# Optimization experiments

Hardware: AMD Instinct MI355X
Metric: run time of the kernel (lower is better)

## Reference

```python
import jax, jax.numpy as jnp
import numpy as np
import itertools

# ---- fixed problem dims ----
B, C, G, D, H, W_SP = 2, 32, 24, 24, 24, 24   # octahedral group |G| = 24 (isomorphic to S4)
N_SEL = 3                                      # selective bispectrum: 2nd shift restricted to {e, transposition, 4-cycle}
FEAT = G * N_SEL                               # 72 invariant features per channel
HEAD = 64


def _octahedral_tables():
    """Cayley table of the octahedral rotation group (== S4) and the selective generator set."""
    perms = list(itertools.permutations(range(4)))          # lexicographic; identity at index 0
    idx = {p: i for i, p in enumerate(perms)}
    # cayley[i, j] = index of p_i o p_j, with (p o q)(k) = p(q(k))
    cay = np.array([[idx[tuple(p[q[k]] for k in range(4))] for q in perms] for p in perms],
                   dtype=np.int32)
    sel = np.array([idx[(0, 1, 2, 3)],   # identity
                    idx[(1, 0, 2, 3)],   # transposition (generator)
                    idx[(1, 2, 3, 0)]],  # 4-cycle (generator)
                   dtype=np.int32)
    return cay, sel


def setup_inputs() -> dict:
    key = jax.random.key(0)
    k1, k2, k3 = jax.random.split(key, 3)
    x = jax.random.normal(k1, (B, C, G, D, H, W_SP), dtype=jnp.float32)
    cay, sel = _octahedral_tables()
    # 1x1x1 Conv3d params: weight (HEAD, C*FEAT), bias (HEAD,)
    fan_in = C * FEAT
    W = jax.random.normal(k2, (HEAD, fan_in), dtype=jnp.float32) * (1.0 / np.sqrt(fan_in))
    b = jax.random.normal(k3, (HEAD,), dtype=jnp.float32) * 0.01
    return {"x": x, "W": W, "b": b,
            "cayley": jnp.asarray(cay), "sel_idx": jnp.asarray(sel)}


def _bispectrum_pool(x, W, b, cayley, sel_idx):
    Bb, Cc, Gg, Dd, Hh, Ww = x.shape
    # (B,C,G,D,H,W) -> rows of group signals, one per (b,c,voxel)
    xf = x.astype(jnp.float32).transpose(0, 1, 3, 4, 5, 2).reshape(-1, Gg)   # (N, 24)
    N = xf.shape[0]
    # Selective triple correlation (bispectrum in group domain):
    #   tau[n, h, s] = sum_g f(g) * f(g.h) * f(g.s),  s in selective generator set
    tau = jnp.zeros((N, Gg, N_SEL), dtype=jnp.float32)
    for g in range(Gg):                      # fixed small loop over 24 group elements
        row = cayley[g]                      # (24,) indices of g.h for all h
        fgh = xf[:, row]                     # (N, 24)
        fgs = fgh[:, sel_idx]                # (N, 3)
        tau = tau + xf[:, g][:, None, None] * fgh[:, :, None] * fgs[:, None, :]
    beta = tau.reshape(N, FEAT)              # real part of the bispectrum
    # sign * log1p compression
    out = jnp.sign(beta) * jnp.log1p(jnp.abs(beta))
    # (N, FEAT) -> (B, C*FEAT, D, H, W), channel index = c*FEAT + f (matches torch permute/reshape)
    out = out.reshape(Bb, Cc, Dd, Hh, Ww, FEAT).transpose(0, 1, 5, 2, 3, 4)
    out = out.reshape(Bb, Cc * FEAT, Dd, Hh, Ww)
    out = jax.nn.relu(out)
    # 1x1x1 conv == per-voxel GEMM
    y = jnp.einsum('bkdhw,ok->bodhw', out, W) + b[None, :, None, None, None]
    return y


def reference(x, W, b, cayley, sel_idx):
    return _bispectrum_pool(x, W, b, cayley, sel_idx)
```

## Files before the change

kernel.cpp:

```cpp
#include <hip/hip_runtime.h>
#include <stdint.h>

#define DHW         13824
#define NCH         32
#define NG          24
#define KDIM        2304
#define NHEAD       64
#define TP          16
#define CHS         16
#define FPC         64
#define KP2         2048
#define KS2         64
#define KPSTG       32
#define KQ          8
#define RPE         1024
#define TILES_PER_B 864
#define NTILES      1728
#define OUTN        1769472
#define WS_WBS      294912
#define WS_NEED     (WS_WBS + 2u * OUTN * 4u)

typedef __attribute__((ext_vector_type(2))) float    f32x2;
typedef __attribute__((ext_vector_type(8))) short    s16x8;
typedef __attribute__((ext_vector_type(4))) float    f32x4;
typedef __attribute__((ext_vector_type(4))) uint32_t u32x4;

struct Tables { int cay[NG][NG]; int s1[NG]; int s2[NG]; int t1h[NG]; int rep[12]; };

constexpr Tables make_tables() {
    int perms[NG][4] = {};
    int n = 0;
    for (int a = 0; a < 4; ++a)
        for (int b = 0; b < 4; ++b) {
            if (b == a) continue;
            for (int c = 0; c < 4; ++c) {
                if (c == a || c == b) continue;
                int d = 6 - a - b - c;
                perms[n][0] = a; perms[n][1] = b; perms[n][2] = c; perms[n][3] = d;
                ++n;
            }
        }
    int si1 = 0, si2 = 0;
    for (int i = 0; i < NG; ++i) {
        if (perms[i][0] == 1 && perms[i][1] == 0 && perms[i][2] == 2 && perms[i][3] == 3) si1 = i;
        if (perms[i][0] == 1 && perms[i][1] == 2 && perms[i][2] == 3 && perms[i][3] == 0) si2 = i;
    }
    Tables t{};
    for (int p = 0; p < NG; ++p) {
        for (int q = 0; q < NG; ++q) {
            int c0 = perms[p][perms[q][0]];
            int c1 = perms[p][perms[q][1]];
            int c2 = perms[p][perms[q][2]];
            int c3 = perms[p][perms[q][3]];
            int r = 0;
            for (int i = 0; i < NG; ++i)
                if (perms[i][0] == c0 && perms[i][1] == c1 &&
                    perms[i][2] == c2 && perms[i][3] == c3) { r = i; break; }
            t.cay[p][q] = r;
        }
        t.s1[p] = t.cay[p][si1];
        t.s2[p] = t.cay[p][si2];
    }
    for (int h = 0; h < NG; ++h) t.t1h[h] = t.cay[si1][h];
    int nr = 0;
    for (int h = 0; h < NG; ++h) if (h < t.t1h[h]) t.rep[nr++] = h;
    return t;
}
constexpr Tables TAB = make_tables();

__device__ __forceinline__ uint32_t f2bf(float f) {
    uint32_t u = __float_as_uint(f);
    u += 0x7fffu + ((u >> 16) & 1u);
    return u >> 16;
}

__global__ __launch_bounds__(256) void prep_w(const float* __restrict__ W,
                                              unsigned short* __restrict__ WbS) {
    int i = blockIdx.x * 256 + threadIdx.x;
    int j  = i & 7;
    int t1_ = i >> 3;
    int l  = t1_ & 63;
    int t2_ = t1_ >> 6;
    int kk = t2_ & (KS2 - 1);
    int ot = t2_ >> 6;
    int o = ot * 16 + (l & 15);
    int k = kk * 32 + ((l >> 4) << 3) + j;
    int stage = k >> 10;
    int q     = k & 1023;
    int c = stage * CHS + (q >> 6);
    int f = q & 63;
    const float* Wo = W + o * KDIM + c * 72;
    float val = 0.f;
    if (f < 24)      val = Wo[f * 3 + 0];
    else if (f < 36) { int h = TAB.rep[f - 24]; val = Wo[h * 3 + 1] + Wo[TAB.t1h[h] * 3 + 1]; }
    else if (f < 60) { int h = f - 36;          val = Wo[h * 3 + 2]; }
    WbS[i] = (unsigned short)f2bf(val * 0.69314718055994531f);
}

__global__ __launch_bounds__(256) void reduce_y(const float* __restrict__ part,
                                                const float* __restrict__ bias,
                                                float* __restrict__ y) {
    const int i4 = blockIdx.x * 256 + threadIdx.x;
    const f32x4 v0 = ((const f32x4*)part)[i4];
    const f32x4 v1 = ((const f32x4*)(part + OUTN))[i4];
    const float b  = bias[((i4 * 4) / DHW) & (NHEAD - 1)];
    f32x4 r = v0 + v1;
    r[0] += b; r[1] += b; r[2] += b; r[3] += b;
    ((f32x4*)y)[i4] = r;
}

template<int SPLIT>
__global__ __launch_bounds__(256, 2)
void bispec_fused(
        const float* __restrict__ x,
        const unsigned short* __restrict__ WbS,
        const float* __restrict__ bias,
        float* __restrict__ out)
{
    __shared__ alignas(16) unsigned short featS[TP * RPE];

    const int bid = blockIdx.x;
    const int NB  = SPLIT ? NTILES * 2 : NTILES;
    const int swz   = (bid & 7) * (NB / 8) + (bid >> 3);
    const int tile  = SPLIT ? (swz % NTILES) : swz;
    const int sbeg  = SPLIT ? (swz / NTILES) : 0;
    const int send  = SPLIT ? sbeg + 1 : 2;
    const int bb  = tile / TILES_PER_B;
    const int psp = (tile - bb * TILES_PER_B) * TP;
    const int tid = threadIdx.x;

    const int p0 = tid & 15;
    const int cl = tid >> 4;
    const int w  = tid >> 6;
    const int l  = tid & 63;
    const int ln = l & 15;
    const int lh = l >> 4;

    f32x4 accA = {0.f, 0.f, 0.f, 0.f};
    f32x4 accB = {0.f, 0.f, 0.f, 0.f};
    f32x4 accC = {0.f, 0.f, 0.f, 0.f};
    f32x4 accD = {0.f, 0.f, 0.f, 0.f};

    #pragma unroll 1
    for (int stage = sbeg; stage < send; ++stage) {
        {
            const int c0 = stage * CHS + cl;
            const unsigned idx0 = (unsigned)(bb * NCH + c0) * (NG * DHW) + (unsigned)(psp + p0);
            float xf[NG];
            #pragma unroll
            for (int g = 0; g < NG; ++g) xf[g] = x[idx0 + (unsigned)(g * DHW)];

            f32x2 tau02[NG];
            float tau1[12];
            #pragma unroll
            for (int h = 0; h < NG; ++h) tau02[h] = (f32x2){0.f, 0.f};
            #pragma unroll
            for (int r = 0; r < 12; ++r) tau1[r] = 0.f;
            #pragma unroll
            for (int g = 0; g < NG; ++g) {
                const float xg = xf[g];
                const f32x2 q02 = (f32x2){xg, xg} * (f32x2){xg, xf[TAB.s2[g]]};
                const float q1 = xg * xf[TAB.s1[g]];
                #pragma unroll
                for (int h = 0; h < NG; ++h) {
                    const float v = xf[TAB.cay[g][h]];
                    tau02[h] = __builtin_elementwise_fma((f32x2){v, v}, q02, tau02[h]);
                }
                #pragma unroll
                for (int r = 0; r < 12; ++r) {
                    const float v = xf[TAB.cay[g][TAB.rep[r]]];
                    tau1[r] = fmaf(q1, v, tau1[r]);
                }
            }
            uint32_t pk[FPC / 2];
            #pragma unroll
            for (int i = 0; i < 12; ++i) {
                float a = __log2f(1.f + fmaxf(tau02[2*i][0],   0.f));
                float b = __log2f(1.f + fmaxf(tau02[2*i+1][0], 0.f));
                pk[i] = f2bf(a) | (f2bf(b) << 16);
            }
            #pragma unroll
            for (int i = 0; i < 6; ++i) {
                float a = __log2f(1.f + fmaxf(tau1[2*i],   0.f));
                float b = __log2f(1.f + fmaxf(tau1[2*i+1], 0.f));
                pk[12 + i] = f2bf(a) | (f2bf(b) << 16);
            }
            #pragma unroll
            for (int i = 0; i < 12; ++i) {
                float a = __log2f(1.f + fmaxf(tau02[2*i][1],   0.f));
                float b = __log2f(1.f + fmaxf(tau02[2*i+1][1], 0.f));
                pk[18 + i] = f2bf(a) | (f2bf(b) << 16);
            }
            pk[30] = 0u; pk[31] = 0u;
            uint32_t* rowb = (uint32_t*)featS + p0 * (RPE / 2);
            #pragma unroll
            for (int j = 0; j < 8; ++j) {
                u32x4 v; v[0] = pk[j*4]; v[1] = pk[j*4+1]; v[2] = pk[j*4+2]; v[3] = pk[j*4+3];
                *(u32x4*)(rowb + ((((cl << 3) + j) ^ (p0 & 7)) << 2)) = v;
            }
        }
        __syncthreads();

        {
            const unsigned kb = (unsigned)(stage * KPSTG + w * KQ);
            const unsigned short* rowr = featS + ln * RPE;
            const int sx = ln & 7;
            const s16x8* wb = (const s16x8*)WbS;

            s16x8 bc = *(const s16x8*)(rowr + (((w * 32 + lh) ^ sx) << 3));
            #pragma unroll
            for (int kk = 0; kk < KQ; ++kk) {
                s16x8 bn = bc;
                if (kk + 1 < KQ)
                    bn = *(const s16x8*)(rowr + (((w * 32 + (kk + 1) * 4 + lh) ^ sx) << 3));
                const unsigned ai = (kb + (unsigned)kk) * 64u + (unsigned)l;
                s16x8 a0 = wb[ai];
                s16x8 a1 = wb[ai + 1u * KS2 * 64u];
                s16x8 a2 = wb[ai + 2u * KS2 * 64u];
                s16x8 a3 = wb[ai + 3u * KS2 * 64u];
                accA = __builtin_amdgcn_mfma_f32_16x16x32_bf16(a0, bc, accA, 0, 0, 0);
                accB = __builtin_amdgcn_mfma_f32_16x16x32_bf16(a1, bc, accB, 0, 0, 0);
                accC = __builtin_amdgcn_mfma_f32_16x16x32_bf16(a2, bc, accC, 0, 0, 0);
                accD = __builtin_amdgcn_mfma_f32_16x16x32_bf16(a3, bc, accD, 0, 0, 0);
                bc = bn;
            }
        }
        __syncthreads();
    }

    f32x4* redS = (f32x4*)featS;
    redS[(w * 4 + 0) * 64 + l] = accA;
    redS[(w * 4 + 1) * 64 + l] = accB;
    redS[(w * 4 + 2) * 64 + l] = accC;
    redS[(w * 4 + 3) * 64 + l] = accD;
    __syncthreads();
    f32x4 r = redS[(0 * 4 + w) * 64 + l] + redS[(1 * 4 + w) * 64 + l]
            + redS[(2 * 4 + w) * 64 + l] + redS[(3 * 4 + w) * 64 + l];

    const size_t obase = (SPLIT ? (size_t)sbeg * OUTN : 0)
                       + (size_t)bb * NHEAD * DHW + (size_t)(psp + ln);
    #pragma unroll
    for (int j = 0; j < 4; ++j) {
        const int o = w * 16 + lh * 4 + j;
        const float bv = SPLIT ? 0.f : bias[o];
        out[obase + (size_t)o * DHW] = r[j] + bv;
    }
}

extern "C" void kernel_launch(void* const* d_in, const int* in_sizes, int n_in,
                              void* d_out, int out_size, void* d_ws, size_t ws_size,
                              hipStream_t stream) {
    const float* x    = (const float*)d_in[0];
    const float* W    = (const float*)d_in[1];
    const float* bias = (const float*)d_in[2];
    unsigned short* WbS = (unsigned short*)d_ws;
    float* part = (float*)((char*)d_ws + WS_WBS);

    prep_w<<<dim3(NHEAD * KP2 / 256), dim3(256), 0, stream>>>(W, WbS);
    if (ws_size >= (size_t)WS_NEED) {
        bispec_fused<1><<<dim3(NTILES * 2), dim3(256), 0, stream>>>(x, WbS, bias, part);
        reduce_y<<<dim3(OUTN / 4 / 256), dim3(256), 0, stream>>>(part, bias, (float*)d_out);
    } else {
        bispec_fused<0><<<dim3(NTILES), dim3(256), 0, stream>>>(x, WbS, bias, (float*)d_out);
    }
}
```

Before: 62.15 us.

## Split channels four ways with half-group threads and atomic output accumulation

```diff
diff --git a/kernel.cpp b/kernel.cpp
--- a/kernel.cpp
+++ b/kernel.cpp
@@ -7,18 +7,18 @@
 #define KDIM        2304
 #define NHEAD       64
 #define TP          16
-#define CHS         16
+#define CHS         8
+#define NSTG        4
 #define FPC         64
 #define KP2         2048
 #define KS2         64
-#define KPSTG       32
-#define KQ          8
-#define RPE         1024
+#define KSTG        16
+#define KQ          4
+#define RPE         512
 #define TILES_PER_B 864
 #define NTILES      1728
+#define NB          (NTILES * NSTG)
 #define OUTN        1769472
-#define WS_WBS      294912
-#define WS_NEED     (WS_WBS + 2u * OUTN * 4u)
 
 typedef __attribute__((ext_vector_type(2))) float    f32x2;
 typedef __attribute__((ext_vector_type(8))) short    s16x8;
@@ -85,148 +85,147 @@
     int ot = t2_ >> 6;
     int o = ot * 16 + (l & 15);
     int k = kk * 32 + ((l >> 4) << 3) + j;
-    int stage = k >> 10;
-    int q     = k & 1023;
-    int c = stage * CHS + (q >> 6);
-    int f = q & 63;
+    int c  = k >> 6;
+    int f  = k & 63;
+    int H  = f >> 5, fl = f & 31;
     const float* Wo = W + o * KDIM + c * 72;
     float val = 0.f;
-    if (f < 24)      val = Wo[f * 3 + 0];
-    else if (f < 36) { int h = TAB.rep[f - 24]; val = Wo[h * 3 + 1] + Wo[TAB.t1h[h] * 3 + 1]; }
-    else if (f < 60) { int h = f - 36;          val = Wo[h * 3 + 2]; }
+    if (fl < 12)      val = Wo[(H * 12 + fl) * 3 + 0];
+    else if (fl < 18) { int h = TAB.rep[H * 6 + fl - 12];
+                        val = Wo[h * 3 + 1] + Wo[TAB.t1h[h] * 3 + 1]; }
+    else if (fl < 30) val = Wo[(H * 12 + fl - 18) * 3 + 2];
     WbS[i] = (unsigned short)f2bf(val * 0.69314718055994531f);
 }
 
-__global__ __launch_bounds__(256) void reduce_y(const float* __restrict__ part,
-                                                const float* __restrict__ bias,
-                                                float* __restrict__ y) {
+__global__ __launch_bounds__(256) void bias_add(float* __restrict__ y,
+                                                const float* __restrict__ bias) {
     const int i4 = blockIdx.x * 256 + threadIdx.x;
-    const f32x4 v0 = ((const f32x4*)part)[i4];
-    const f32x4 v1 = ((const f32x4*)(part + OUTN))[i4];
-    const float b  = bias[((i4 * 4) / DHW) & (NHEAD - 1)];
-    f32x4 r = v0 + v1;
-    r[0] += b; r[1] += b; r[2] += b; r[3] += b;
-    ((f32x4*)y)[i4] = r;
-}
-
-template<int SPLIT>
+    f32x4 v = ((f32x4*)y)[i4];
+    const float b = bias[((i4 * 4) / DHW) & (NHEAD - 1)];
+    v[0] += b; v[1] += b; v[2] += b; v[3] += b;
+    ((f32x4*)y)[i4] = v;
+}
+
+template<int H>
+__device__ __forceinline__ void half_core(const float (&xf)[NG],
+                                          f32x2 (&tau02)[12], float (&tau1)[6]) {
+    #pragma unroll
+    for (int i = 0; i < 12; ++i) tau02[i] = (f32x2){0.f, 0.f};
+    #pragma unroll
+    for (int i = 0; i < 6; ++i) tau1[i] = 0.f;
+    #pragma unroll
+    for (int g = 0; g < NG; ++g) {
+        const float xg = xf[g];
+        const f32x2 q02 = (f32x2){xg, xg} * (f32x2){xg, xf[TAB.s2[g]]};
+        const float q1 = xg * xf[TAB.s1[g]];
+        #pragma unroll
+        for (int hh = 0; hh < 12; ++hh) {
+            const float v = xf[TAB.cay[g][H * 12 + hh]];
+            tau02[hh] = __builtin_elementwise_fma((f32x2){v, v}, q02, tau02[hh]);
+        }
+        #pragma unroll
+        for (int rr = 0; rr < 6; ++rr) {
+            const float v = xf[TAB.cay[g][TAB.rep[H * 6 + rr]]];
+            tau1[rr] = fmaf(q1, v, tau1[rr]);
+        }
+    }
+}
+
 __global__ __launch_bounds__(256, 2)
 void bispec_fused(
         const float* __restrict__ x,
         const unsigned short* __restrict__ WbS,
-        const float* __restrict__ bias,
-        float* __restrict__ out)
+        float* __restrict__ y)
 {
     __shared__ alignas(16) unsigned short featS[TP * RPE];
 
     const int bid = blockIdx.x;
-    const int NB  = SPLIT ? NTILES * 2 : NTILES;
-    const int swz   = (bid & 7) * (NB / 8) + (bid >> 3);
-    const int tile  = SPLIT ? (swz % NTILES) : swz;
-    const int sbeg  = SPLIT ? (swz / NTILES) : 0;
-    const int send  = SPLIT ? sbeg + 1 : 2;
+    const int swz  = (bid & 7) * (NB / 8) + (bid >> 3);
+    const int tile = swz >> 2;
+    const int cs   = swz & 3;
     const int bb  = tile / TILES_PER_B;
     const int psp = (tile - bb * TILES_PER_B) * TP;
     const int tid = threadIdx.x;
 
     const int p0 = tid & 15;
-    const int cl = tid >> 4;
+    const int cl = (tid >> 4) & 7;
+    const int H  = tid >> 7;
     const int w  = tid >> 6;
     const int l  = tid & 63;
     const int ln = l & 15;
     const int lh = l >> 4;
 
+    {
+        const int c0 = cs * CHS + cl;
+        const unsigned idx0 = (unsigned)(bb * NCH + c0) * (NG * DHW) + (unsigned)(psp + p0);
+        float xf[NG];
+        #pragma unroll
+        for (int g = 0; g < NG; ++g) xf[g] = x[idx0 + (unsigned)(g * DHW)];
+
+        f32x2 tau02[12];
+        float tau1[6];
+        if (tid < 128) half_core<0>(xf, tau02, tau1);
+        else           half_core<1>(xf, tau02, tau1);
+
+        uint32_t pk[16];
+        #pragma unroll
+        for (int i = 0; i < 6; ++i) {
+            float a = __log2f(1.f + fmaxf(tau02[2*i][0],   0.f));
+            float b = __log2f(1.f + fmaxf(tau02[2*i+1][0], 0.f));
+            pk[i] = f2bf(a) | (f2bf(b) << 16);
+        }
+        #pragma unroll
+        for (int i = 0; i < 3; ++i) {
+            float a = __log2f(1.f + fmaxf(tau1[2*i],   0.f));
+            float b = __log2f(1.f + fmaxf(tau1[2*i+1], 0.f));
+            pk[6 + i] = f2bf(a) | (f2bf(b) << 16);
+        }
+        #pragma unroll
+        for (int i = 0; i < 6; ++i) {
+            float a = __log2f(1.f + fmaxf(tau02[2*i][1],   0.f));
+            float b = __log2f(1.f + fmaxf(tau02[2*i+1][1], 0.f));
+            pk[9 + i] = f2bf(a) | (f2bf(b) << 16);
+        }
+        pk[15] = 0u;
+        uint32_t* rowb = (uint32_t*)featS + p0 * (RPE / 2);
+        const int cb = cl * 8 + H * 4;
+        #pragma unroll
+        for (int j = 0; j < 4; ++j) {
+            u32x4 v; v[0] = pk[j*4]; v[1] = pk[j*4+1]; v[2] = pk[j*4+2]; v[3] = pk[j*4+3];
+            *(u32x4*)(rowb + (((cb + j) ^ (p0 & 7)) << 2)) = v;
+        }
+    }
+    __syncthreads();
+
     f32x4 accA = {0.f, 0.f, 0.f, 0.f};
     f32x4 accB = {0.f, 0.f, 0.f, 0.f};
     f32x4 accC = {0.f, 0.f, 0.f, 0.f};
     f32x4 accD = {0.f, 0.f, 0.f, 0.f};
-
-    #pragma unroll 1
-    for (int stage = sbeg; stage < send; ++stage) {
-        {
-            const int c0 = stage * CHS + cl;
-            const unsigned idx0 = (unsigned)(bb * NCH + c0) * (NG * DHW) + (unsigned)(psp + p0);
-            float xf[NG];
-            #pragma unroll
-            for (int g = 0; g < NG; ++g) xf[g] = x[idx0 + (unsigned)(g * DHW)];
-
-            f32x2 tau02[NG];
-            float tau1[12];
-            #pragma unroll
-            for (int h = 0; h < NG; ++h) tau02[h] = (f32x2){0.f, 0.f};
-            #pragma unroll
-            for (int r = 0; r < 12; ++r) tau1[r] = 0.f;
-            #pragma unroll
-            for (int g = 0; g < NG; ++g) {
-                const float xg = xf[g];
-                const f32x2 q02 = (f32x2){xg, xg} * (f32x2){xg, xf[TAB.s2[g]]};
-                const float q1 = xg * xf[TAB.s1[g]];
-                #pragma unroll
-                for (int h = 0; h < NG; ++h) {
-                    const float v = xf[TAB.cay[g][h]];
-                    tau02[h] = __builtin_elementwise_fma((f32x2){v, v}, q02, tau02[h]);
-                }
-                #pragma unroll
-                for (int r = 0; r < 12; ++r) {
-                    const float v = xf[TAB.cay[g][TAB.rep[r]]];
-                    tau1[r] = fmaf(q1, v, tau1[r]);
-                }
-            }
-            uint32_t pk[FPC / 2];
-            #pragma unroll
-            for (int i = 0; i < 12; ++i) {
-                float a = __log2f(1.f + fmaxf(tau02[2*i][0],   0.f));
-                float b = __log2f(1.f + fmaxf(tau02[2*i+1][0], 0.f));
-                pk[i] = f2bf(a) | (f2bf(b) << 16);
-            }
-            #pragma unroll
-            for (int i = 0; i < 6; ++i) {
-                float a = __log2f(1.f + fmaxf(tau1[2*i],   0.f));
-                float b = __log2f(1.f + fmaxf(tau1[2*i+1], 0.f));
-                pk[12 + i] = f2bf(a) | (f2bf(b) << 16);
-            }
-            #pragma unroll
-            for (int i = 0; i < 12; ++i) {
-                float a = __log2f(1.f + fmaxf(tau02[2*i][1],   0.f));
-                float b = __log2f(1.f + fmaxf(tau02[2*i+1][1], 0.f));
-                pk[18 + i] = f2bf(a) | (f2bf(b) << 16);
-            }
-            pk[30] = 0u; pk[31] = 0u;
-            uint32_t* rowb = (uint32_t*)featS + p0 * (RPE / 2);
-            #pragma unroll
-            for (int j = 0; j < 8; ++j) {
-                u32x4 v; v[0] = pk[j*4]; v[1] = pk[j*4+1]; v[2] = pk[j*4+2]; v[3] = pk[j*4+3];
-                *(u32x4*)(rowb + ((((cl << 3) + j) ^ (p0 & 7)) << 2)) = v;
-            }
-        }
-        __syncthreads();
-
-        {
-            const unsigned kb = (unsigned)(stage * KPSTG + w * KQ);
-            const unsigned short* rowr = featS + ln * RPE;
-            const int sx = ln & 7;
-            const s16x8* wb = (const s16x8*)WbS;
-
-            s16x8 bc = *(const s16x8*)(rowr + (((w * 32 + lh) ^ sx) << 3));
-            #pragma unroll
-            for (int kk = 0; kk < KQ; ++kk) {
-                s16x8 bn = bc;
-                if (kk + 1 < KQ)
-                    bn = *(const s16x8*)(rowr + (((w * 32 + (kk + 1) * 4 + lh) ^ sx) << 3));
-                const unsigned ai = (kb + (unsigned)kk) * 64u + (unsigned)l;
-                s16x8 a0 = wb[ai];
-                s16x8 a1 = wb[ai + 1u * KS2 * 64u];
-                s16x8 a2 = wb[ai + 2u * KS2 * 64u];
-                s16x8 a3 = wb[ai + 3u * KS2 * 64u];
-                accA = __builtin_amdgcn_mfma_f32_16x16x32_bf16(a0, bc, accA, 0, 0, 0);
-                accB = __builtin_amdgcn_mfma_f32_16x16x32_bf16(a1, bc, accB, 0, 0, 0);
-                accC = __builtin_amdgcn_mfma_f32_16x16x32_bf16(a2, bc, accC, 0, 0, 0);
-                accD = __builtin_amdgcn_mfma_f32_16x16x32_bf16(a3, bc, accD, 0, 0, 0);
-                bc = bn;
-            }
-        }
-        __syncthreads();
-    }
+    {
+        const unsigned kb = (unsigned)(cs * KSTG + w * KQ);
+        const unsigned short* rowr = featS + ln * RPE;
+        const int sx = ln & 7;
+        const s16x8* wb = (const s16x8*)WbS;
+
+        s16x8 bc = *(const s16x8*)(rowr + (((w * 16 + lh) ^ sx) << 3));
+        #pragma unroll
+        for (int kk = 0; kk < KQ; ++kk) {
+            s16x8 bn = bc;
+            if (kk + 1 < KQ)
+                bn = *(const s16x8*)(rowr + (((w * 16 + (kk + 1) * 4 + lh) ^ sx) << 3));
+            const unsigned ai = (kb + (unsigned)kk) * 64u + (unsigned)l;
+            s16x8 a0 = wb[ai];
+            s16x8 a1 = wb[ai + 1u * KS2 * 64u];
+            s16x8 a2 = wb[ai + 2u * KS2 * 64u];
+            s16x8 a3 = wb[ai + 3u * KS2 * 64u];
+            accA = __builtin_amdgcn_mfma_f32_16x16x32_bf16(a0, bc, accA, 0, 0, 0);
+            accB = __builtin_amdgcn_mfma_f32_16x16x32_bf16(a1, bc, accB, 0, 0, 0);
+            accC = __builtin_amdgcn_mfma_f32_16x16x32_bf16(a2, bc, accC, 0, 0, 0);
+            accD = __builtin_amdgcn_mfma_f32_16x16x32_bf16(a3, bc, accD, 0, 0, 0);
+            bc = bn;
+        }
+    }
+    __syncthreads();
 
     f32x4* redS = (f32x4*)featS;
     redS[(w * 4 + 0) * 64 + l] = accA;
@@ -237,13 +236,11 @@
     f32x4 r = redS[(0 * 4 + w) * 64 + l] + redS[(1 * 4 + w) * 64 + l]
             + redS[(2 * 4 + w) * 64 + l] + redS[(3 * 4 + w) * 64 + l];
 
-    const size_t obase = (SPLIT ? (size_t)sbeg * OUTN : 0)
-                       + (size_t)bb * NHEAD * DHW + (size_t)(psp + ln);
+    const size_t obase = (size_t)bb * NHEAD * DHW + (size_t)(psp + ln);
     #pragma unroll
     for (int j = 0; j < 4; ++j) {
         const int o = w * 16 + lh * 4 + j;
-        const float bv = SPLIT ? 0.f : bias[o];
-        out[obase + (size_t)o * DHW] = r[j] + bv;
+        atomicAdd(&y[obase + (size_t)o * DHW], r[j]);
     }
 }
 
@@ -254,13 +251,10 @@
     const float* W    = (const float*)d_in[1];
     const float* bias = (const float*)d_in[2];
     unsigned short* WbS = (unsigned short*)d_ws;
-    float* part = (float*)((char*)d_ws + WS_WBS);
+    float* y = (float*)d_out;
 
     prep_w<<<dim3(NHEAD * KP2 / 256), dim3(256), 0, stream>>>(W, WbS);
-    if (ws_size >= (size_t)WS_NEED) {
-        bispec_fused<1><<<dim3(NTILES * 2), dim3(256), 0, stream>>>(x, WbS, bias, part);
-        reduce_y<<<dim3(OUTN / 4 / 256), dim3(256), 0, stream>>>(part, bias, (float*)d_out);
-    } else {
-        bispec_fused<0><<<dim3(NTILES), dim3(256), 0, stream>>>(x, WbS, bias, (float*)d_out);
-    }
-}
+    hipMemsetAsync(y, 0, (size_t)OUTN * sizeof(float), stream);
+    bispec_fused<<<dim3(NB), dim3(256), 0, stream>>>(x, WbS, y);
+    bias_add<<<dim3(OUTN / 4 / 256), dim3(256), 0, stream>>>(y, bias);
+}
```

After: 67.60 us. 1.09x slower.
